# Performance work log

Hardware: AMD Instinct MI355X
Metric: run time of the kernel (lower is better)

## Reference

```python
import jax, jax.numpy as jnp
import numpy as np

D_MODEL = 768
HEADS = 12
D_K = D_MODEL // HEADS
NEG = -1e9


def setup_inputs() -> dict:
    key = jax.random.key(0)
    ks = jax.random.split(key, 7)
    B, S, D = 4, 2048, D_MODEL
    scale = 1.0 / np.sqrt(D)
    q = jax.random.normal(ks[0], (B, S, D), dtype=jnp.float32)
    k = jax.random.normal(ks[1], (B, S, D), dtype=jnp.float32)
    v = jax.random.normal(ks[2], (B, S, D), dtype=jnp.float32)
    # causal mask, broadcastable over batch and heads; mask==0 -> -1e9
    mask = jnp.tril(jnp.ones((1, 1, S, S), dtype=jnp.int32))
    W_q = jax.random.normal(ks[3], (D, D), dtype=jnp.float32) * scale
    W_k = jax.random.normal(ks[4], (D, D), dtype=jnp.float32) * scale
    W_v = jax.random.normal(ks[5], (D, D), dtype=jnp.float32) * scale
    W_o = jax.random.normal(ks[6], (D, D), dtype=jnp.float32) * scale
    return {"q": q, "k": k, "v": v, "mask": mask,
            "W_q": W_q, "W_k": W_k, "W_v": W_v, "W_o": W_o}


def reference(q, k, v, mask, W_q, W_k, W_v, W_o):
    B, S, D = q.shape
    # nn.Linear(bias=False): y = x @ W.T
    query = (q @ W_q.T).reshape(B, S, HEADS, D_K).transpose(0, 2, 1, 3)  # [B,H,S,dk]
    key_ = (k @ W_k.T).reshape(B, S, HEADS, D_K).transpose(0, 2, 1, 3)
    value = (v @ W_v.T).reshape(B, S, HEADS, D_K).transpose(0, 2, 1, 3)
    scores = jnp.einsum('bhqd,bhkd->bhqk', query, key_) / jnp.sqrt(
        jnp.asarray(D_K, dtype=query.dtype))
    scores = jnp.where(mask == 0, jnp.asarray(NEG, dtype=scores.dtype), scores)
    attn = jax.nn.softmax(scores, axis=-1)
    # dropout rate = 0.0 (inference / eval mode): identity
    x = jnp.einsum('bhqk,bhkd->bhqd', attn, value)  # [B,H,S,dk]
    x = x.transpose(0, 2, 1, 3).reshape(B, S, D)
    return x @ W_o.T
```

## Files before the change

### kernel.cpp

```cpp
#include <hip/hip_runtime.h>


typedef _Float16 f16x8 __attribute__((ext_vector_type(8)));
typedef _Float16 f16x4 __attribute__((ext_vector_type(4)));
typedef float floatx4 __attribute__((ext_vector_type(4)));

#define MFMA16(a, b, c) __builtin_amdgcn_mfma_f32_16x16x32_f16((a), (b), (c), 0, 0, 0)

static constexpr int B_ = 4;
static constexpr int S_ = 2048;
static constexpr int D_ = 768;
static constexpr int H_ = 12;
static constexpr int DK = 64;

__device__ __forceinline__ f16x8 cvt8(float4 a, float4 b) {
  f16x8 h;
  h[0] = (_Float16)a.x; h[1] = (_Float16)a.y;
  h[2] = (_Float16)a.z; h[3] = (_Float16)a.w;
  h[4] = (_Float16)b.x; h[5] = (_Float16)b.y;
  h[6] = (_Float16)b.z; h[7] = (_Float16)b.w;
  return h;
}

__device__ __forceinline__ void dma16(const _Float16* g, _Float16* l) {
  __builtin_amdgcn_global_load_lds(
      (const __attribute__((address_space(1))) unsigned int*)g,
      (__attribute__((address_space(3))) unsigned int*)l, 16, 0, 0);
}

struct CvtArgs {
  const float* src[4];
  _Float16* dst[4];
  int end[4];
  int nseg;
};

__global__ __launch_bounds__(256) void cvt_f32_f16(CvtArgs a) {
  int b = blockIdx.x;
  int s = 0;
  while (s < a.nseg - 1 && b >= a.end[s]) ++s;
  int local = b - (s ? a.end[s - 1] : 0);
  const int tid = threadIdx.x;
  const float4* p = (const float4*)(a.src[s] + (size_t)local * 2048) + tid * 2;
  float4 x0 = p[0], x1 = p[1];
  *(f16x8*)(a.dst[s] + (size_t)local * 2048 + tid * 8) = cvt8(x0, x1);
}

static constexpr int PAN = 128 * 32;

struct QkvPtrs {
  const void* a[3];
  const void* w[3];
};

__global__ __launch_bounds__(256) void qkv_f32a(QkvPtrs P, _Float16* Qh,
                                                _Float16* Kh, _Float16* Vt) {
  __shared__ _Float16 As[2 * PAN];
  __shared__ _Float16 Bs[2 * PAN];
  constexpr int K = 768;

  const int z = blockIdx.z;
  const float* A = (const float*)P.a[z];
  const _Float16* W = (const _Float16*)P.w[z];

  const int tid = threadIdx.x;
  const int wave = tid >> 6, lane = tid & 63;
  const int l15 = lane & 15, quad = lane >> 4;
  const int wm = (wave >> 1) * 64, wn = (wave & 1) * 64;
  const int m0 = blockIdx.y * 128, n0 = blockIdx.x * 128;
  const int lr = lane >> 2, lc = (lane & 3) * 8;

  floatx4 acc[4][4] = {};

  for (int k0 = 0; k0 < K; k0 += 64) {
    {
      const _Float16* g = W + (size_t)(n0 + wave * 16 + lr) * K + k0 + lc;
      dma16(g, Bs + wave * 16 * 32);
      dma16(g + 32, Bs + PAN + wave * 16 * 32);
      const _Float16* g2 = g + (size_t)64 * K;
      dma16(g2, Bs + (64 + wave * 16) * 32);
      dma16(g2 + 32, Bs + PAN + (64 + wave * 16) * 32);
    }
#pragma unroll
    for (int jj = 0; jj < 4; ++jj) {
      int flat8 = jj * 256 + tid;
      int row = flat8 >> 3;
      int k8 = flat8 & 7;
      const float4* p =
          (const float4*)(A + (size_t)(m0 + row) * K + k0 + k8 * 8);
      float4 x0 = p[0], x1 = p[1];
      *(f16x8*)(As + (k8 >> 2) * PAN + row * 32 + (k8 & 3) * 8) = cvt8(x0, x1);
    }
    __syncthreads();

#pragma unroll
    for (int p = 0; p < 2; ++p) {
      f16x8 af[4], bf[4];
#pragma unroll
      for (int t = 0; t < 4; ++t)
        af[t] = *(const f16x8*)(As + p * PAN + (wm + t * 16 + l15) * 32 +
                                quad * 8);
#pragma unroll
      for (int t = 0; t < 4; ++t)
        bf[t] = *(const f16x8*)(Bs + p * PAN + (wn + t * 16 + l15) * 32 +
                                quad * 8);
#pragma unroll
      for (int mt = 0; mt < 4; ++mt)
#pragma unroll
        for (int nt = 0; nt < 4; ++nt)
          acc[mt][nt] = MFMA16(af[mt], bf[nt], acc[mt][nt]);
    }
    __syncthreads();
  }

  const float scale = (z == 0) ? 0.125f : 1.0f;
  if (z < 2) {
    _Float16* C = z ? Kh : Qh;
#pragma unroll
    for (int mt = 0; mt < 4; ++mt)
#pragma unroll
      for (int nt = 0; nt < 4; ++nt)
#pragma unroll
        for (int r = 0; r < 4; ++r) {
          int row = m0 + wm + mt * 16 + quad * 4 + r;
          int col = n0 + wn + nt * 16 + l15;
          int b = row >> 11, s = row & 2047;
          int h = col >> 6, d = col & 63;
          C[((size_t)(b * H_ + h) * S_ + s) * DK + d] =
              (_Float16)(acc[mt][nt][r] * scale);
        }
  } else {
#pragma unroll
    for (int mt = 0; mt < 4; ++mt)
#pragma unroll
      for (int nt = 0; nt < 4; ++nt) {
        int row = m0 + wm + mt * 16 + quad * 4;
        int col = n0 + wn + nt * 16 + l15;
        int b = row >> 11, s = row & 2047;
        int h = col >> 6, d = col & 63;
        f16x4 v4;
#pragma unroll
        for (int r = 0; r < 4; ++r) v4[r] = (_Float16)acc[mt][nt][r];
        *(f16x4*)(Vt + ((size_t)(b * H_ + h) * DK + d) * S_ + s) = v4;
      }
  }
}

static constexpr int PAN_A = 64 * 32;
static constexpr int PAN_B = 128 * 32;

__global__ __launch_bounds__(256) void gemm_o64(const _Float16* __restrict__ A,
                                                const _Float16* __restrict__ W,
                                                float* __restrict__ C) {
  __shared__ _Float16 As[2 * PAN_A];
  __shared__ _Float16 Bs[2 * PAN_B];
  constexpr int K = 768;
  constexpr int N = 768;

  const int tid = threadIdx.x;
  const int wave = tid >> 6, lane = tid & 63;
  const int l15 = lane & 15, quad = lane >> 4;
  const int wm = (wave >> 1) * 32, wn = (wave & 1) * 64;
  const int m0 = blockIdx.y * 64, n0 = blockIdx.x * 128;
  const int lr = lane >> 2, lc = (lane & 3) * 8;

  floatx4 acc[2][4] = {};

  for (int k0 = 0; k0 < K; k0 += 64) {
#pragma unroll
    for (int p = 0; p < 2; ++p) {
      const _Float16* g =
          A + (size_t)(m0 + wave * 16 + lr) * K + k0 + p * 32 + lc;
      dma16(g, As + p * PAN_A + wave * 16 * 32);
    }
#pragma unroll
    for (int p = 0; p < 2; ++p)
#pragma unroll
      for (int q = 0; q < 2; ++q) {
        const _Float16* g =
            W + (size_t)(n0 + wave * 32 + q * 16 + lr) * K + k0 + p * 32 + lc;
        dma16(g, Bs + p * PAN_B + (wave * 32 + q * 16) * 32);
      }
    __syncthreads();

#pragma unroll
    for (int p = 0; p < 2; ++p) {
      f16x8 af[2], bf[4];
#pragma unroll
      for (int t = 0; t < 2; ++t)
        af[t] = *(const f16x8*)(As + p * PAN_A + (wm + t * 16 + l15) * 32 +
                                quad * 8);
#pragma unroll
      for (int t = 0; t < 4; ++t)
        bf[t] = *(const f16x8*)(Bs + p * PAN_B + (wn + t * 16 + l15) * 32 +
                                quad * 8);
#pragma unroll
      for (int mt = 0; mt < 2; ++mt)
#pragma unroll
        for (int nt = 0; nt < 4; ++nt)
          acc[mt][nt] = MFMA16(af[mt], bf[nt], acc[mt][nt]);
    }
    __syncthreads();
  }

#pragma unroll
  for (int mt = 0; mt < 2; ++mt)
#pragma unroll
    for (int nt = 0; nt < 4; ++nt)
#pragma unroll
      for (int r = 0; r < 4; ++r) {
        int row = m0 + wm + mt * 16 + quad * 4 + r;
        int col = n0 + wn + nt * 16 + l15;
        C[(size_t)row * N + col] = acc[mt][nt][r];
      }
}

template <int MODE, bool SCALE>
__global__ __launch_bounds__(256) void gemm128(const float* __restrict__ Av,
                                               const float* __restrict__ Bv,
                                               void* __restrict__ Cv, int M,
                                               int N, int K) {
  __shared__ _Float16 As[128 * 40];
  __shared__ _Float16 Bs[128 * 40];

  const int tid = threadIdx.x;
  const int wave = tid >> 6, lane = tid & 63;
  const int l15 = lane & 15, quad = lane >> 4;
  const int wm = (wave >> 1) * 64, wn = (wave & 1) * 64;
  const int m0 = blockIdx.y * 128, n0 = blockIdx.x * 128;
  const int srow = tid >> 1, scol = (tid & 1) * 16;

  floatx4 acc[4][4] = {};

  for (int k0 = 0; k0 < K; k0 += 32) {
    {
      const float4* p =
          (const float4*)(Av + (size_t)(m0 + srow) * K + k0 + scol);
      float4 x0 = p[0], x1 = p[1], x2 = p[2], x3 = p[3];
      *(f16x8*)(As + srow * 40 + scol) = cvt8(x0, x1);
      *(f16x8*)(As + srow * 40 + scol + 8) = cvt8(x2, x3);
    }
    {
      const float4* p =
          (const float4*)(Bv + (size_t)(n0 + srow) * K + k0 + scol);
      float4 x0 = p[0], x1 = p[1], x2 = p[2], x3 = p[3];
      *(f16x8*)(Bs + srow * 40 + scol) = cvt8(x0, x1);
      *(f16x8*)(Bs + srow * 40 + scol + 8) = cvt8(x2, x3);
    }
    __syncthreads();

    f16x8 af[4], bf[4];
#pragma unroll
    for (int t = 0; t < 4; ++t)
      af[t] = *(const f16x8*)(As + (wm + t * 16 + l15) * 40 + quad * 8);
#pragma unroll
    for (int t = 0; t < 4; ++t)
      bf[t] = *(const f16x8*)(Bs + (wn + t * 16 + l15) * 40 + quad * 8);
#pragma unroll
    for (int mt = 0; mt < 4; ++mt)
#pragma unroll
      for (int nt = 0; nt < 4; ++nt)
        acc[mt][nt] = MFMA16(af[mt], bf[nt], acc[mt][nt]);
    __syncthreads();
  }

#pragma unroll
  for (int mt = 0; mt < 4; ++mt)
#pragma unroll
    for (int nt = 0; nt < 4; ++nt)
#pragma unroll
      for (int r = 0; r < 4; ++r) {
        int row = m0 + wm + mt * 16 + quad * 4 + r;
        int col = n0 + wn + nt * 16 + l15;
        float val = acc[mt][nt][r];
        if constexpr (SCALE) val *= 0.125f;
        if constexpr (MODE == 0) {
          ((float*)Cv)[(size_t)row * N + col] = val;
        } else if constexpr (MODE == 1) {
          int b = row >> 11, s = row & 2047;
          int h = col >> 6, d = col & 63;
          ((_Float16*)Cv)[((size_t)(b * H_ + h) * S_ + s) * DK + d] =
              (_Float16)val;
        } else {
          int b = col >> 11, s = col & 2047;
          int h = row >> 6, d = row & 63;
          ((_Float16*)Cv)[((size_t)(b * H_ + h) * DK + d) * S_ + s] =
              (_Float16)val;
        }
      }
}

__global__ __launch_bounds__(256) void gemm_out_f32w(
    const _Float16* __restrict__ A, const float* __restrict__ Bv,
    float* __restrict__ C) {
  __shared__ _Float16 As[128 * 40];
  __shared__ _Float16 Bs[128 * 40];
  constexpr int K = 768, N = 768;

  const int tid = threadIdx.x;
  const int wave = tid >> 6, lane = tid & 63;
  const int l15 = lane & 15, quad = lane >> 4;
  const int wm = (wave >> 1) * 64, wn = (wave & 1) * 64;
  const int m0 = blockIdx.y * 128, n0 = blockIdx.x * 128;
  const int srow = tid >> 1, scol = (tid & 1) * 16;

  floatx4 acc[4][4] = {};

  for (int k0 = 0; k0 < K; k0 += 32) {
    {
      const f16x8* p = (const f16x8*)(A + (size_t)(m0 + srow) * K + k0 + scol);
      *(f16x8*)(As + srow * 40 + scol) = p[0];
      *(f16x8*)(As + srow * 40 + scol + 8) = p[1];
    }
    {
      const float4* p =
          (const float4*)(Bv + (size_t)(n0 + srow) * K + k0 + scol);
      float4 x0 = p[0], x1 = p[1], x2 = p[2], x3 = p[3];
      *(f16x8*)(Bs + srow * 40 + scol) = cvt8(x0, x1);
      *(f16x8*)(Bs + srow * 40 + scol + 8) = cvt8(x2, x3);
    }
    __syncthreads();

    f16x8 af[4], bf[4];
#pragma unroll
    for (int t = 0; t < 4; ++t)
      af[t] = *(const f16x8*)(As + (wm + t * 16 + l15) * 40 + quad * 8);
#pragma unroll
    for (int t = 0; t < 4; ++t)
      bf[t] = *(const f16x8*)(Bs + (wn + t * 16 + l15) * 40 + quad * 8);
#pragma unroll
    for (int mt = 0; mt < 4; ++mt)
#pragma unroll
      for (int nt = 0; nt < 4; ++nt)
        acc[mt][nt] = MFMA16(af[mt], bf[nt], acc[mt][nt]);
    __syncthreads();
  }

#pragma unroll
  for (int mt = 0; mt < 4; ++mt)
#pragma unroll
    for (int nt = 0; nt < 4; ++nt)
#pragma unroll
      for (int r = 0; r < 4; ++r) {
        int row = m0 + wm + mt * 16 + quad * 4 + r;
        int col = n0 + wn + nt * 16 + l15;
        C[(size_t)row * N + col] = acc[mt][nt][r];
      }
}

__global__ __launch_bounds__(256, 3) void flash_attn(
    const _Float16* __restrict__ Qh, const _Float16* __restrict__ Kh,
    const _Float16* __restrict__ Vt, _Float16* __restrict__ Oh) {
  __shared__ _Float16 Ks[64 * 72];
  __shared__ _Float16 Vts[64 * 72];
  __shared__ _Float16 Ps[4][16 * 36];

  const int tid = threadIdx.x;
  const int wave = tid >> 6, lane = tid & 63;
  const int l15 = lane & 15, quad = lane >> 4;

  const int linear = blockIdx.x + gridDim.x * blockIdx.y;
  const int xcd = linear & 7;
  const int seq = linear >> 3;
  const int bh = xcd * 6 + (seq >> 4);
  const int qt = 15 - (seq & 15);
  const int b = bh / H_, h = bh % H_;
  const int q0 = qt * 128;
  const size_t base = (size_t)bh * S_ * DK;
  const size_t basev = (size_t)bh * DK * S_;

  f16x8 qf[2][2];
#pragma unroll
  for (int mt = 0; mt < 2; ++mt) {
    int qrow = q0 + mt * 64 + wave * 16 + l15;
    qf[mt][0] = *(const f16x8*)(Qh + base + (size_t)qrow * DK + quad * 8);
    qf[mt][1] = *(const f16x8*)(Qh + base + (size_t)qrow * DK + 32 + quad * 8);
  }

  floatx4 o_acc[2][4] = {};
  float plsum[2][4] = {};

  const int srow = tid >> 2;
  const int sc0 = (tid & 3) * 16;
  const int jmax = 2 * qt + 1;

  const _Float16* ks = Kh + base + (size_t)srow * DK + sc0;
  const _Float16* vs = Vt + basev + (size_t)srow * S_ + sc0;
  f16x8 pk0 = *(const f16x8*)ks;
  f16x8 pk1 = *(const f16x8*)(ks + 8);
  f16x8 pv0 = *(const f16x8*)vs;
  f16x8 pv1 = *(const f16x8*)(vs + 8);

  for (int j = 0; j <= jmax; ++j) {
    const int j0 = j * 64;
    __syncthreads();
    *(f16x8*)(Ks + srow * 72 + sc0) = pk0;
    *(f16x8*)(Ks + srow * 72 + sc0 + 8) = pk1;
    *(f16x8*)(Vts + srow * 72 + sc0) = pv0;
    *(f16x8*)(Vts + srow * 72 + sc0 + 8) = pv1;
    __syncthreads();

    if (j < jmax) {
      const _Float16* kn = Kh + base + (size_t)((j + 1) * 64 + srow) * DK + sc0;
      const _Float16* vn = Vt + basev + (size_t)srow * S_ + (j + 1) * 64 + sc0;
      pk0 = *(const f16x8*)kn;
      pk1 = *(const f16x8*)(kn + 8);
      pv0 = *(const f16x8*)vn;
      pv1 = *(const f16x8*)(vn + 8);
    }

#pragma unroll
    for (int mt = 0; mt < 2; ++mt) {
      const int rbase = q0 + mt * 64 + wave * 16;
      if (j0 > rbase + 15) continue;

      floatx4 s_acc[4] = {};
#pragma unroll
      for (int t = 0; t < 4; ++t) {
        f16x8 kf0 = *(const f16x8*)(Ks + (t * 16 + l15) * 72 + quad * 8);
        f16x8 kf1 = *(const f16x8*)(Ks + (t * 16 + l15) * 72 + 32 + quad * 8);
        s_acc[t] = MFMA16(qf[mt][0], kf0, s_acc[t]);
        s_acc[t] = MFMA16(qf[mt][1], kf1, s_acc[t]);
      }

      const bool need_mask = (j0 + 63 > rbase);
      float p[4][4];
#pragma unroll
      for (int t = 0; t < 4; ++t)
#pragma unroll
        for (int r = 0; r < 4; ++r) {
          float s = s_acc[t][r];
          if (need_mask) {
            int rg = rbase + quad * 4 + r;
            int cg = j0 + t * 16 + l15;
            if (cg > rg) s = -1e30f;
          }
          float e = __expf(s);
          p[t][r] = e;
          plsum[mt][r] += e;
        }

#pragma unroll
      for (int t = 0; t < 2; ++t)
#pragma unroll
        for (int r = 0; r < 4; ++r)
          Ps[wave][(quad * 4 + r) * 36 + t * 16 + l15] = (_Float16)p[t][r];
      f16x8 pf0 = *(const f16x8*)(Ps[wave] + l15 * 36 + quad * 8);
#pragma unroll
      for (int t = 0; t < 4; ++t) {
        f16x8 vf0 = *(const f16x8*)(Vts + (t * 16 + l15) * 72 + quad * 8);
        o_acc[mt][t] = MFMA16(pf0, vf0, o_acc[mt][t]);
      }
#pragma unroll
      for (int t = 2; t < 4; ++t)
#pragma unroll
        for (int r = 0; r < 4; ++r)
          Ps[wave][(quad * 4 + r) * 36 + (t - 2) * 16 + l15] =
              (_Float16)p[t][r];
      f16x8 pf1 = *(const f16x8*)(Ps[wave] + l15 * 36 + quad * 8);
#pragma unroll
      for (int t = 0; t < 4; ++t) {
        f16x8 vf1 = *(const f16x8*)(Vts + (t * 16 + l15) * 72 + 32 + quad * 8);
        o_acc[mt][t] = MFMA16(pf1, vf1, o_acc[mt][t]);
      }
    }
  }

#pragma unroll
  for (int mt = 0; mt < 2; ++mt)
#pragma unroll
    for (int r = 0; r < 4; ++r) {
      float l = plsum[mt][r];
      l += __shfl_xor(l, 1);
      l += __shfl_xor(l, 2);
      l += __shfl_xor(l, 4);
      l += __shfl_xor(l, 8);
      float inv = 1.0f / l;
      int row = q0 + mt * 64 + wave * 16 + quad * 4 + r;
#pragma unroll
      for (int t = 0; t < 4; ++t) {
        float val = o_acc[mt][t][r] * inv;
        Oh[((size_t)(b * S_ + row)) * D_ + h * DK + t * 16 + l15] =
            (_Float16)val;
      }
    }
}

extern "C" void kernel_launch(void* const* d_in, const int* in_sizes, int n_in,
                              void* d_out, int out_size, void* d_ws,
                              size_t ws_size, hipStream_t stream) {
  const float* q = (const float*)d_in[0];
  const float* k = (const float*)d_in[1];
  const float* v = (const float*)d_in[2];
  const float* Wq = (const float*)d_in[4];
  const float* Wk = (const float*)d_in[5];
  const float* Wv = (const float*)d_in[6];
  const float* Wo = (const float*)d_in[7];
  float* out = (float*)d_out;

  const size_t E = (size_t)B_ * H_ * S_ * DK;
  const size_t EW = (size_t)D_ * D_;
  _Float16* Qh = (_Float16*)d_ws;
  _Float16* Kh = Qh + E;
  _Float16* Vt = Kh + E;
  _Float16* Oh = Vt + E;

  const int M = B_ * S_;
  dim3 blk(256);
  dim3 qg(D_ / 128, M / 128, 3);
  dim3 og(D_ / 128, M / 64);
  dim3 pg(D_ / 128, M / 128);
  dim3 fg(16, B_ * H_);

  const size_t need_w = (4 * E + 4 * EW) * 2;

  if (ws_size >= need_w) {
    _Float16* wqf = Oh + E;
    _Float16* wkf = wqf + EW;
    _Float16* wvf = wkf + EW;
    _Float16* wof = wvf + EW;
    CvtArgs ca;
    ca.src[0] = Wq; ca.dst[0] = wqf;
    ca.src[1] = Wk; ca.dst[1] = wkf;
    ca.src[2] = Wv; ca.dst[2] = wvf;
    ca.src[3] = Wo; ca.dst[3] = wof;
    int ends[4] = {288, 576, 864, 1152};
    for (int i = 0; i < 4; ++i) ca.end[i] = ends[i];
    ca.nseg = 4;
    cvt_f32_f16<<<1152, blk, 0, stream>>>(ca);
    QkvPtrs P;
    P.a[0] = q; P.a[1] = k; P.a[2] = v;
    P.w[0] = wqf; P.w[1] = wkf; P.w[2] = wvf;
    qkv_f32a<<<qg, blk, 0, stream>>>(P, Qh, Kh, Vt);
    flash_attn<<<fg, blk, 0, stream>>>(Qh, Kh, Vt, Oh);
    gemm_o64<<<og, blk, 0, stream>>>(Oh, wof, out);
  } else {
    gemm128<1, true><<<pg, blk, 0, stream>>>(q, Wq, Qh, M, D_, D_);
    gemm128<1, false><<<pg, blk, 0, stream>>>(k, Wk, Kh, M, D_, D_);
    gemm128<2, false><<<dim3(M / 128, D_ / 128), blk, 0, stream>>>(
        Wv, v, Vt, D_, M, D_);
    flash_attn<<<fg, blk, 0, stream>>>(Qh, Kh, Vt, Oh);
    gemm_out_f32w<<<pg, blk, 0, stream>>>(Oh, Wo, out);
  }
}
```

Baseline: 304.7 us.

## Pre-convert activations to fp16, DMA both GEMM operands, pair causal tiles in attention

After: 280.8 us. 1.08x faster.

```diff
diff --git a/kernel.cpp b/kernel.cpp
--- a/kernel.cpp
+++ b/kernel.cpp
@@ -29,9 +29,9 @@
 }
 
 struct CvtArgs {
-  const float* src[4];
-  _Float16* dst[4];
-  int end[4];
+  const float* src[7];
+  _Float16* dst[7];
+  int end[7];
   int nseg;
 };
 
@@ -53,43 +53,38 @@
   const void* w[3];
 };
 
-__global__ __launch_bounds__(256) void qkv_f32a(QkvPtrs P, _Float16* Qh,
-                                                _Float16* Kh, _Float16* Vt) {
-  __shared__ _Float16 As[2 * PAN];
-  __shared__ _Float16 Bs[2 * PAN];
-  constexpr int K = 768;
-
-  const int z = blockIdx.z;
-  const float* A = (const float*)P.a[z];
-  const _Float16* W = (const _Float16*)P.w[z];
-
+template <int MODE, bool SCALE>
+__device__ __forceinline__ void gemm_core64(const _Float16* __restrict__ A,
+                                            const _Float16* __restrict__ Bm,
+                                            void* __restrict__ Cv,
+                                            _Float16* As, _Float16* Bs,
+                                            int m0, int n0, int N, int K) {
   const int tid = threadIdx.x;
   const int wave = tid >> 6, lane = tid & 63;
   const int l15 = lane & 15, quad = lane >> 4;
   const int wm = (wave >> 1) * 64, wn = (wave & 1) * 64;
-  const int m0 = blockIdx.y * 128, n0 = blockIdx.x * 128;
-  const int lr = lane >> 2, lc = (lane & 3) * 8;
+  const int lr = lane >> 2;
+  const int lc = (lane & 3) * 8;
+  const int wb = wave * 16;
 
   floatx4 acc[4][4] = {};
 
   for (int k0 = 0; k0 < K; k0 += 64) {
     {
-      const _Float16* g = W + (size_t)(n0 + wave * 16 + lr) * K + k0 + lc;
-      dma16(g, Bs + wave * 16 * 32);
-      dma16(g + 32, Bs + PAN + wave * 16 * 32);
+      const _Float16* g = A + (size_t)(m0 + wb + lr) * K + k0 + lc;
+      dma16(g, As + wb * 32);
+      dma16(g + 32, As + PAN + wb * 32);
       const _Float16* g2 = g + (size_t)64 * K;
-      dma16(g2, Bs + (64 + wave * 16) * 32);
-      dma16(g2 + 32, Bs + PAN + (64 + wave * 16) * 32);
-    }
-#pragma unroll
-    for (int jj = 0; jj < 4; ++jj) {
-      int flat8 = jj * 256 + tid;
-      int row = flat8 >> 3;
-      int k8 = flat8 & 7;
-      const float4* p =
-          (const float4*)(A + (size_t)(m0 + row) * K + k0 + k8 * 8);
-      float4 x0 = p[0], x1 = p[1];
-      *(f16x8*)(As + (k8 >> 2) * PAN + row * 32 + (k8 & 3) * 8) = cvt8(x0, x1);
+      dma16(g2, As + (64 + wb) * 32);
+      dma16(g2 + 32, As + PAN + (64 + wb) * 32);
+    }
+    {
+      const _Float16* g = Bm + (size_t)(n0 + wb + lr) * K + k0 + lc;
+      dma16(g, Bs + wb * 32);
+      dma16(g + 32, Bs + PAN + wb * 32);
+      const _Float16* g2 = g + (size_t)64 * K;
+      dma16(g2, Bs + (64 + wb) * 32);
+      dma16(g2 + 32, Bs + PAN + (64 + wb) * 32);
     }
     __syncthreads();
 
@@ -113,23 +108,7 @@
     __syncthreads();
   }
 
-  const float scale = (z == 0) ? 0.125f : 1.0f;
-  if (z < 2) {
-    _Float16* C = z ? Kh : Qh;
-#pragma unroll
-    for (int mt = 0; mt < 4; ++mt)
-#pragma unroll
-      for (int nt = 0; nt < 4; ++nt)
-#pragma unroll
-        for (int r = 0; r < 4; ++r) {
-          int row = m0 + wm + mt * 16 + quad * 4 + r;
-          int col = n0 + wn + nt * 16 + l15;
-          int b = row >> 11, s = row & 2047;
-          int h = col >> 6, d = col & 63;
-          C[((size_t)(b * H_ + h) * S_ + s) * DK + d] =
-              (_Float16)(acc[mt][nt][r] * scale);
-        }
-  } else {
+  if constexpr (MODE == 2) {
 #pragma unroll
     for (int mt = 0; mt < 4; ++mt)
 #pragma unroll
@@ -141,8 +120,47 @@
         f16x4 v4;
 #pragma unroll
         for (int r = 0; r < 4; ++r) v4[r] = (_Float16)acc[mt][nt][r];
-        *(f16x4*)(Vt + ((size_t)(b * H_ + h) * DK + d) * S_ + s) = v4;
-      }
+        *(f16x4*)((_Float16*)Cv + ((size_t)(b * H_ + h) * DK + d) * S_ + s) =
+            v4;
+      }
+  } else {
+#pragma unroll
+    for (int mt = 0; mt < 4; ++mt)
+#pragma unroll
+      for (int nt = 0; nt < 4; ++nt)
+#pragma unroll
+        for (int r = 0; r < 4; ++r) {
+          int row = m0 + wm + mt * 16 + quad * 4 + r;
+          int col = n0 + wn + nt * 16 + l15;
+          float val = acc[mt][nt][r];
+          if constexpr (SCALE) val *= 0.125f;
+          if constexpr (MODE == 0) {
+            ((float*)Cv)[(size_t)row * N + col] = val;
+          } else {
+            int b = row >> 11, s = row & 2047;
+            int h = col >> 6, d = col & 63;
+            ((_Float16*)Cv)[((size_t)(b * H_ + h) * S_ + s) * DK + d] =
+                (_Float16)val;
+          }
+        }
+  }
+}
+
+__global__ __launch_bounds__(256) void qkv_gemm64(QkvPtrs P, _Float16* Qh,
+                                                  _Float16* Kh, _Float16* Vt) {
+  __shared__ _Float16 As[2 * PAN];
+  __shared__ _Float16 Bs[2 * PAN];
+  const int z = blockIdx.z;
+  const int m0 = blockIdx.y * 128, n0 = blockIdx.x * 128;
+  if (z == 0) {
+    gemm_core64<1, true>((const _Float16*)P.a[0], (const _Float16*)P.w[0], Qh,
+                         As, Bs, m0, n0, D_, D_);
+  } else if (z == 1) {
+    gemm_core64<1, false>((const _Float16*)P.a[1], (const _Float16*)P.w[1], Kh,
+                          As, Bs, m0, n0, D_, D_);
+  } else {
+    gemm_core64<2, false>((const _Float16*)P.a[2], (const _Float16*)P.w[2], Vt,
+                          As, Bs, m0, n0, D_, D_);
   }
 }
 
@@ -154,8 +172,7 @@
                                                 float* __restrict__ C) {
   __shared__ _Float16 As[2 * PAN_A];
   __shared__ _Float16 Bs[2 * PAN_B];
-  constexpr int K = 768;
-  constexpr int N = 768;
+  constexpr int K = 768, N = 768;
 
   const int tid = threadIdx.x;
   const int wave = tid >> 6, lane = tid & 63;
@@ -213,6 +230,166 @@
         int col = n0 + wn + nt * 16 + l15;
         C[(size_t)row * N + col] = acc[mt][nt][r];
       }
+}
+
+__global__ __launch_bounds__(256, 3) void flash_attn(
+    const _Float16* __restrict__ Qh, const _Float16* __restrict__ Kh,
+    const _Float16* __restrict__ Vt, _Float16* __restrict__ Oh) {
+  __shared__ _Float16 Ks[64 * 72];
+  __shared__ _Float16 Vts[64 * 72];
+  __shared__ _Float16 Ps[4][16 * 36];
+
+  const int tid = threadIdx.x;
+  const int wave = tid >> 6, lane = tid & 63;
+  const int l15 = lane & 15, quad = lane >> 4;
+
+  const int linear = blockIdx.x + gridDim.x * blockIdx.y;
+  const int xcd = linear & 7;
+  const int seq = linear >> 3;
+  const int bh = xcd * 6 + (seq >> 3);
+  const int x = seq & 7;
+  const int b = bh / H_, h = bh % H_;
+  const size_t base = (size_t)bh * S_ * DK;
+  const size_t basev = (size_t)bh * DK * S_;
+
+  const int srow = tid >> 2;
+  const int sc0 = (tid & 3) * 16;
+
+  for (int c = 0; c < 2; ++c) {
+    const int qt = c ? x : 15 - x;
+    const int q0 = qt * 128;
+    const int jmax = 2 * qt + 1;
+
+    f16x8 qf[2][2];
+#pragma unroll
+    for (int mt = 0; mt < 2; ++mt) {
+      int qrow = q0 + mt * 64 + wave * 16 + l15;
+      qf[mt][0] = *(const f16x8*)(Qh + base + (size_t)qrow * DK + quad * 8);
+      qf[mt][1] =
+          *(const f16x8*)(Qh + base + (size_t)qrow * DK + 32 + quad * 8);
+    }
+
+    floatx4 o_acc[2][4] = {};
+    float plsum[2][4] = {};
+
+    const _Float16* ks = Kh + base + (size_t)srow * DK + sc0;
+    const _Float16* vs = Vt + basev + (size_t)srow * S_ + sc0;
+    f16x8 pk0 = *(const f16x8*)ks;
+    f16x8 pk1 = *(const f16x8*)(ks + 8);
+    f16x8 pv0 = *(const f16x8*)vs;
+    f16x8 pv1 = *(const f16x8*)(vs + 8);
+
+    for (int j = 0; j <= jmax; ++j) {
+      const int j0 = j * 64;
+      __syncthreads();
+      *(f16x8*)(Ks + srow * 72 + sc0) = pk0;
+      *(f16x8*)(Ks + srow * 72 + sc0 + 8) = pk1;
+      *(f16x8*)(Vts + srow * 72 + sc0) = pv0;
+      *(f16x8*)(Vts + srow * 72 + sc0 + 8) = pv1;
+      __syncthreads();
+
+      if (j < jmax) {
+        const _Float16* kn =
+            Kh + base + (size_t)((j + 1) * 64 + srow) * DK + sc0;
+        const _Float16* vn =
+            Vt + basev + (size_t)srow * S_ + (j + 1) * 64 + sc0;
+        pk0 = *(const f16x8*)kn;
+        pk1 = *(const f16x8*)(kn + 8);
+        pv0 = *(const f16x8*)vn;
+        pv1 = *(const f16x8*)(vn + 8);
+      }
+
+      const int rb0 = q0 + wave * 16;
+      const int rb1 = q0 + 64 + wave * 16;
+      const bool a0 = (j0 <= rb0 + 15);
+      const bool a1 = (j0 <= rb1 + 15);
+
+      floatx4 s_acc[2][4] = {};
+#pragma unroll
+      for (int t = 0; t < 4; ++t) {
+        f16x8 kf0 = *(const f16x8*)(Ks + (t * 16 + l15) * 72 + quad * 8);
+        f16x8 kf1 = *(const f16x8*)(Ks + (t * 16 + l15) * 72 + 32 + quad * 8);
+        if (a0) {
+          s_acc[0][t] = MFMA16(qf[0][0], kf0, s_acc[0][t]);
+          s_acc[0][t] = MFMA16(qf[0][1], kf1, s_acc[0][t]);
+        }
+        if (a1) {
+          s_acc[1][t] = MFMA16(qf[1][0], kf0, s_acc[1][t]);
+          s_acc[1][t] = MFMA16(qf[1][1], kf1, s_acc[1][t]);
+        }
+      }
+
+      f16x8 pf[2][2];
+#pragma unroll
+      for (int mt = 0; mt < 2; ++mt) {
+        const bool act = mt ? a1 : a0;
+        if (!act) continue;
+        const int rbase = mt ? rb1 : rb0;
+        const bool need_mask = (j0 + 63 > rbase);
+        float p[4][4];
+#pragma unroll
+        for (int t = 0; t < 4; ++t)
+#pragma unroll
+          for (int r = 0; r < 4; ++r) {
+            float s = s_acc[mt][t][r];
+            if (need_mask) {
+              int rg = rbase + quad * 4 + r;
+              int cg = j0 + t * 16 + l15;
+              if (cg > rg) s = -1e30f;
+            }
+            float e = __expf(s);
+            p[t][r] = e;
+            plsum[mt][r] += e;
+          }
+#pragma unroll
+        for (int t = 0; t < 2; ++t)
+#pragma unroll
+          for (int r = 0; r < 4; ++r)
+            Ps[wave][(quad * 4 + r) * 36 + t * 16 + l15] = (_Float16)p[t][r];
+        pf[mt][0] = *(const f16x8*)(Ps[wave] + l15 * 36 + quad * 8);
+#pragma unroll
+        for (int t = 2; t < 4; ++t)
+#pragma unroll
+          for (int r = 0; r < 4; ++r)
+            Ps[wave][(quad * 4 + r) * 36 + (t - 2) * 16 + l15] =
+                (_Float16)p[t][r];
+        pf[mt][1] = *(const f16x8*)(Ps[wave] + l15 * 36 + quad * 8);
+      }
+
+#pragma unroll
+      for (int t = 0; t < 4; ++t) {
+        f16x8 vf0 = *(const f16x8*)(Vts + (t * 16 + l15) * 72 + quad * 8);
+        f16x8 vf1 = *(const f16x8*)(Vts + (t * 16 + l15) * 72 + 32 + quad * 8);
+        if (a0) {
+          o_acc[0][t] = MFMA16(pf[0][0], vf0, o_acc[0][t]);
+          o_acc[0][t] = MFMA16(pf[0][1], vf1, o_acc[0][t]);
+        }
+        if (a1) {
+          o_acc[1][t] = MFMA16(pf[1][0], vf0, o_acc[1][t]);
+          o_acc[1][t] = MFMA16(pf[1][1], vf1, o_acc[1][t]);
+        }
+      }
+    }
+
+#pragma unroll
+    for (int mt = 0; mt < 2; ++mt)
+#pragma unroll
+      for (int r = 0; r < 4; ++r) {
+        float l = plsum[mt][r];
+        l += __shfl_xor(l, 1);
+        l += __shfl_xor(l, 2);
+        l += __shfl_xor(l, 4);
+        l += __shfl_xor(l, 8);
+        float inv = 1.0f / l;
+        int row = q0 + mt * 64 + wave * 16 + quad * 4 + r;
+#pragma unroll
+        for (int t = 0; t < 4; ++t) {
+          float val = o_acc[mt][t][r] * inv;
+          Oh[((size_t)(b * S_ + row)) * D_ + h * DK + t * 16 + l15] =
+              (_Float16)val;
+        }
+      }
+  }
 }
 
 template <int MODE, bool SCALE>
@@ -348,144 +525,6 @@
       }
 }
 
-__global__ __launch_bounds__(256, 3) void flash_attn(
-    const _Float16* __restrict__ Qh, const _Float16* __restrict__ Kh,
-    const _Float16* __restrict__ Vt, _Float16* __restrict__ Oh) {
-  __shared__ _Float16 Ks[64 * 72];
-  __shared__ _Float16 Vts[64 * 72];
-  __shared__ _Float16 Ps[4][16 * 36];
-
-  const int tid = threadIdx.x;
-  const int wave = tid >> 6, lane = tid & 63;
-  const int l15 = lane & 15, quad = lane >> 4;
-
-  const int linear = blockIdx.x + gridDim.x * blockIdx.y;
-  const int xcd = linear & 7;
-  const int seq = linear >> 3;
-  const int bh = xcd * 6 + (seq >> 4);
-  const int qt = 15 - (seq & 15);
-  const int b = bh / H_, h = bh % H_;
-  const int q0 = qt * 128;
-  const size_t base = (size_t)bh * S_ * DK;
-  const size_t basev = (size_t)bh * DK * S_;
-
-  f16x8 qf[2][2];
-#pragma unroll
-  for (int mt = 0; mt < 2; ++mt) {
-    int qrow = q0 + mt * 64 + wave * 16 + l15;
-    qf[mt][0] = *(const f16x8*)(Qh + base + (size_t)qrow * DK + quad * 8);
-    qf[mt][1] = *(const f16x8*)(Qh + base + (size_t)qrow * DK + 32 + quad * 8);
-  }
-
-  floatx4 o_acc[2][4] = {};
-  float plsum[2][4] = {};
-
-  const int srow = tid >> 2;
-  const int sc0 = (tid & 3) * 16;
-  const int jmax = 2 * qt + 1;
-
-  const _Float16* ks = Kh + base + (size_t)srow * DK + sc0;
-  const _Float16* vs = Vt + basev + (size_t)srow * S_ + sc0;
-  f16x8 pk0 = *(const f16x8*)ks;
-  f16x8 pk1 = *(const f16x8*)(ks + 8);
-  f16x8 pv0 = *(const f16x8*)vs;
-  f16x8 pv1 = *(const f16x8*)(vs + 8);
-
-  for (int j = 0; j <= jmax; ++j) {
-    const int j0 = j * 64;
-    __syncthreads();
-    *(f16x8*)(Ks + srow * 72 + sc0) = pk0;
-    *(f16x8*)(Ks + srow * 72 + sc0 + 8) = pk1;
-    *(f16x8*)(Vts + srow * 72 + sc0) = pv0;
-    *(f16x8*)(Vts + srow * 72 + sc0 + 8) = pv1;
-    __syncthreads();
-
-    if (j < jmax) {
-      const _Float16* kn = Kh + base + (size_t)((j + 1) * 64 + srow) * DK + sc0;
-      const _Float16* vn = Vt + basev + (size_t)srow * S_ + (j + 1) * 64 + sc0;
-      pk0 = *(const f16x8*)kn;
-      pk1 = *(const f16x8*)(kn + 8);
-      pv0 = *(const f16x8*)vn;
-      pv1 = *(const f16x8*)(vn + 8);
-    }
-
-#pragma unroll
-    for (int mt = 0; mt < 2; ++mt) {
-      const int rbase = q0 + mt * 64 + wave * 16;
-      if (j0 > rbase + 15) continue;
-
-      floatx4 s_acc[4] = {};
-#pragma unroll
-      for (int t = 0; t < 4; ++t) {
-        f16x8 kf0 = *(const f16x8*)(Ks + (t * 16 + l15) * 72 + quad * 8);
-        f16x8 kf1 = *(const f16x8*)(Ks + (t * 16 + l15) * 72 + 32 + quad * 8);
-        s_acc[t] = MFMA16(qf[mt][0], kf0, s_acc[t]);
-        s_acc[t] = MFMA16(qf[mt][1], kf1, s_acc[t]);
-      }
-
-      const bool need_mask = (j0 + 63 > rbase);
-      float p[4][4];
-#pragma unroll
-      for (int t = 0; t < 4; ++t)
-#pragma unroll
-        for (int r = 0; r < 4; ++r) {
-          float s = s_acc[t][r];
-          if (need_mask) {
-            int rg = rbase + quad * 4 + r;
-            int cg = j0 + t * 16 + l15;
-            if (cg > rg) s = -1e30f;
-          }
-          float e = __expf(s);
-          p[t][r] = e;
-          plsum[mt][r] += e;
-        }
-
-#pragma unroll
-      for (int t = 0; t < 2; ++t)
-#pragma unroll
-        for (int r = 0; r < 4; ++r)
-          Ps[wave][(quad * 4 + r) * 36 + t * 16 + l15] = (_Float16)p[t][r];
-      f16x8 pf0 = *(const f16x8*)(Ps[wave] + l15 * 36 + quad * 8);
-#pragma unroll
-      for (int t = 0; t < 4; ++t) {
-        f16x8 vf0 = *(const f16x8*)(Vts + (t * 16 + l15) * 72 + quad * 8);
-        o_acc[mt][t] = MFMA16(pf0, vf0, o_acc[mt][t]);
-      }
-#pragma unroll
-      for (int t = 2; t < 4; ++t)
-#pragma unroll
-        for (int r = 0; r < 4; ++r)
-          Ps[wave][(quad * 4 + r) * 36 + (t - 2) * 16 + l15] =
-              (_Float16)p[t][r];
-      f16x8 pf1 = *(const f16x8*)(Ps[wave] + l15 * 36 + quad * 8);
-#pragma unroll
-      for (int t = 0; t < 4; ++t) {
-        f16x8 vf1 = *(const f16x8*)(Vts + (t * 16 + l15) * 72 + 32 + quad * 8);
-        o_acc[mt][t] = MFMA16(pf1, vf1, o_acc[mt][t]);
-      }
-    }
-  }
-
-#pragma unroll
-  for (int mt = 0; mt < 2; ++mt)
-#pragma unroll
-    for (int r = 0; r < 4; ++r) {
-      float l = plsum[mt][r];
-      l += __shfl_xor(l, 1);
-      l += __shfl_xor(l, 2);
-      l += __shfl_xor(l, 4);
-      l += __shfl_xor(l, 8);
-      float inv = 1.0f / l;
-      int row = q0 + mt * 64 + wave * 16 + quad * 4 + r;
-#pragma unroll
-      for (int t = 0; t < 4; ++t) {
-        float val = o_acc[mt][t][r] * inv;
-        Oh[((size_t)(b * S_ + row)) * D_ + h * DK + t * 16 + l15] =
-            (_Float16)val;
-      }
-    }
-}
-
 extern "C" void kernel_launch(void* const* d_in, const int* in_sizes, int n_in,
                               void* d_out, int out_size, void* d_ws,
                               size_t ws_size, hipStream_t stream) {
@@ -510,28 +549,34 @@
   dim3 qg(D_ / 128, M / 128, 3);
   dim3 og(D_ / 128, M / 64);
   dim3 pg(D_ / 128, M / 128);
-  dim3 fg(16, B_ * H_);
-
-  const size_t need_w = (4 * E + 4 * EW) * 2;
-
-  if (ws_size >= need_w) {
-    _Float16* wqf = Oh + E;
+  dim3 fg(8, B_ * H_);
+
+  const size_t need_full = (7 * E + 4 * EW) * 2;
+
+  if (ws_size >= need_full) {
+    _Float16* qf = Oh + E;
+    _Float16* kf = qf + E;
+    _Float16* vf = kf + E;
+    _Float16* wqf = vf + E;
     _Float16* wkf = wqf + EW;
     _Float16* wvf = wkf + EW;
     _Float16* wof = wvf + EW;
     CvtArgs ca;
-    ca.src[0] = Wq; ca.dst[0] = wqf;
-    ca.src[1] = Wk; ca.dst[1] = wkf;
-    ca.src[2] = Wv; ca.dst[2] = wvf;
-    ca.src[3] = Wo; ca.dst[3] = wof;
-    int ends[4] = {288, 576, 864, 1152};
-    for (int i = 0; i < 4; ++i) ca.end[i] = ends[i];
-    ca.nseg = 4;
-    cvt_f32_f16<<<1152, blk, 0, stream>>>(ca);
+    ca.src[0] = q;  ca.dst[0] = qf;
+    ca.src[1] = k;  ca.dst[1] = kf;
+    ca.src[2] = v;  ca.dst[2] = vf;
+    ca.src[3] = Wq; ca.dst[3] = wqf;
+    ca.src[4] = Wk; ca.dst[4] = wkf;
+    ca.src[5] = Wv; ca.dst[5] = wvf;
+    ca.src[6] = Wo; ca.dst[6] = wof;
+    int ends[7] = {3072, 6144, 9216, 9504, 9792, 10080, 10368};
+    for (int i = 0; i < 7; ++i) ca.end[i] = ends[i];
+    ca.nseg = 7;
+    cvt_f32_f16<<<10368, blk, 0, stream>>>(ca);
     QkvPtrs P;
-    P.a[0] = q; P.a[1] = k; P.a[2] = v;
+    P.a[0] = qf; P.a[1] = kf; P.a[2] = vf;
     P.w[0] = wqf; P.w[1] = wkf; P.w[2] = wvf;
-    qkv_f32a<<<qg, blk, 0, stream>>>(P, Qh, Kh, Vt);
+    qkv_gemm64<<<qg, blk, 0, stream>>>(P, Qh, Kh, Vt);
     flash_attn<<<fg, blk, 0, stream>>>(Qh, Kh, Vt, Oh);
     gemm_o64<<<og, blk, 0, stream>>>(Oh, wof, out);
   } else {
```
